# Kernel tuning notes

Measured on AMD Instinct MI355X. Metric: run time of the kernel, lower is better.

Reference implementation:

```python
import jax, jax.numpy as jnp
from jax import lax
import numpy as np

N, I, O = 64, 8, 8
B = 512
S_EX, S_PHI, S_RHO = 10, 60, 60  # S_phi must equal S_rho (alpha loops feed S_rho-sized h into the GRUs)
N_ACTIONS, N_ROLES = 5, 7


def _gru(x, h, Wih, Whh, bih, bhh):
    # torch.nn.GRUCell math
    gi = x @ Wih.T + bih
    gh = h @ Whh.T + bhh
    ir, iz, inn = jnp.split(gi, 3, axis=-1)
    hr, hz, hn = jnp.split(gh, 3, axis=-1)
    r = jax.nn.sigmoid(ir + hr)
    zg = jax.nn.sigmoid(iz + hz)
    n = jnp.tanh(inn + r * hn)
    return (1.0 - zg) * n + zg * h


def setup_inputs() -> dict:
    key = jax.random.key(0)
    ks = jax.random.split(key, 24)
    f32 = jnp.float32
    z = jax.random.normal(ks[0], (B, N, S_EX), f32)
    dz = jax.random.normal(ks[1], (B, N, S_EX), f32)
    has = (jax.random.uniform(ks[2], (B, N)) < 0.9).astype(f32)
    adj = (jnp.triu(jax.random.uniform(ks[3], (N, N)), 1) > 0.7).astype(jnp.int32)

    def lin(k, o, i):
        return (jax.random.normal(k, (o, i), f32) * np.float32(1.0 / np.sqrt(i)))

    d = dict(z=z, dz=dz, has=has, adj=adj)
    d['Wih_f'] = lin(ks[4], 3 * S_PHI, S_RHO)
    d['Whh_f'] = lin(ks[5], 3 * S_PHI, S_PHI)
    d['bih_f'] = jax.random.normal(ks[6], (3 * S_PHI,), f32) * 0.02
    d['bhh_f'] = jax.random.normal(ks[7], (3 * S_PHI,), f32) * 0.02
    d['Wih_b'] = lin(ks[8], 3 * S_PHI, S_RHO)
    d['Whh_b'] = lin(ks[9], 3 * S_PHI, S_PHI)
    d['bih_b'] = jax.random.normal(ks[10], (3 * S_PHI,), f32) * 0.02
    d['bhh_b'] = jax.random.normal(ks[11], (3 * S_PHI,), f32) * 0.02
    d['Wf'] = lin(ks[12], S_RHO, S_PHI + 2 * S_EX)
    d['bf'] = jax.random.normal(ks[13], (S_RHO,), f32) * 0.02
    d['Wb'] = lin(ks[14], S_RHO, S_PHI + 2 * S_EX)
    d['bb'] = jax.random.normal(ks[15], (S_RHO,), f32) * 0.02
    d['Wa'] = lin(ks[16], N_ACTIONS, 2 * S_PHI)
    d['ba'] = jax.random.normal(ks[17], (N_ACTIONS,), f32) * 0.02
    d['Wc'] = lin(ks[18], 1, 2 * S_PHI)
    d['bc'] = jax.random.normal(ks[19], (1,), f32) * 0.02
    d['Wu'] = lin(ks[20], N_ROLES, 2 * S_RHO)
    d['bu'] = jax.random.normal(ks[21], (N_ROLES,), f32) * 0.02
    return d


def reference(z, dz, has, adj,
              Wih_f, Whh_f, bih_f, bhh_f,
              Wih_b, Whh_b, bih_b, bhh_b,
              Wf, bf, Wb, bb, Wa, ba, Wc, bc, Wu, bu):
    Bn, Nn = has.shape
    dt = z.dtype
    adjf = adj.astype(dt)

    # ---- forward sweep over nodes in ascending order ----
    def fwd_outer(rho, i):
        def inner(h, j):
            hn = _gru(rho[j], h, Wih_f, Whh_f, bih_f, bhh_f)
            blend = adjf[j, i] * has[:, j][:, None]  # edge exists AND source node present
            return h + blend * (hn - h), None
        h, _ = lax.scan(inner, jnp.zeros((Bn, S_PHI), dt), jnp.arange(Nn))
        rho_i = jnp.tanh(jnp.concatenate([h, z[:, i], dz[:, i]], 1) @ Wf.T + bf)
        return rho.at[i].set(rho_i), None

    rho_f, _ = lax.scan(fwd_outer, jnp.zeros((Nn, Bn, S_RHO), dt), jnp.arange(Nn))

    # ---- backward sweep over nodes in descending order ----
    def bwd_outer(rho, i):
        def inner(h, j):
            hn = _gru(rho[j], h, Wih_b, Whh_b, bih_b, bhh_b)
            blend = adjf[i, j] * has[:, j][:, None]  # out-edges of i, visited descending
            return h + blend * (hn - h), None
        h, _ = lax.scan(inner, jnp.zeros((Bn, S_PHI), dt), jnp.arange(Nn - 1, -1, -1))
        rho_i = jnp.concatenate([h, z[:, i], dz[:, i]], 1) @ Wb.T + bb
        return rho.at[i].set(rho_i), None

    rho_b, _ = lax.scan(bwd_outer, jnp.zeros((Nn, Bn, S_RHO), dt), jnp.arange(Nn - 1, -1, -1))

    # ---- aggregate outputs (last O nodes) and inputs (first I nodes) ----
    h = jnp.zeros((Bn, S_RHO), dt)
    for i in range(N - O, N):
        hn = _gru(rho_f[i], h, Wih_f, Whh_f, bih_f, bhh_f)
        h = h + has[:, i][:, None] * (hn - h)
    alpha_f = h
    h = jnp.zeros((Bn, S_RHO), dt)
    for i in reversed(range(I)):
        hn = _gru(rho_b[i], h, Wih_b, Whh_b, bih_b, bhh_b)
        h = h + has[:, i][:, None] * (hn - h)
    alpha_b = h

    ab = jnp.concatenate([alpha_f, alpha_b], 1)
    omega = ab @ Wa.T + ba          # [B, 5]
    value = ab @ Wc.T + bc          # [B, 1]

    feats = jnp.concatenate([rho_f, rho_b], -1)           # [N, B, 2*S_rho]
    psi = jnp.einsum('nbs,rs->brn', feats, Wu) + bu[None, :, None]  # [B, 7, N]
    m = has[:, None, :]
    psi = -60.0 * (1.0 - m) + psi * m  # interpolate(-60, psi, has)

    instr_prob = jax.nn.softmax(omega, axis=1)
    role_prob = jax.nn.softmax(psi, axis=2)
    return instr_prob, role_prob, value
```

## Files before the change

### kernel.cpp

```cpp
#include <hip/hip_runtime.h>
#include <hip/hip_bf16.h>

#define NN 64
#define BATCH 512
#define SP 60
#define SG 180
#define SEX 10
#define CATD 80
#define NA 5
#define NR 7
#define OO 8
#define II 8

typedef unsigned long long u64;
typedef unsigned short u16;
typedef unsigned int u32;
typedef unsigned char u8;

#define OFF_Z     0
#define OFF_DZ    327680
#define OFF_HAS   655360
#define OFF_WIHF  688128
#define OFF_WHHF  698928
#define OFF_BIHF  709728
#define OFF_BHHF  709908
#define OFF_WIHB  710088
#define OFF_WHHB  720888
#define OFF_BIHB  731688
#define OFF_BHHB  731868
#define OFF_WF    732048
#define OFF_BF    736848
#define OFF_WB    736908
#define OFF_BB    741708
#define OFF_WA    741768
#define OFF_BA    742368
#define OFF_WC    742373
#define OFF_BC    742493
#define OFF_WU    742494
#define OFF_BU    743334
#define CONV_TOTAL 743341
#define OFF_FLAG  743342
#define OFF_RHOF  743344
#define OFF_RHOB  (OFF_RHOF + 1966080)
#define OFF_ALF   (OFF_RHOB + 1966080)
#define OFF_ALB   (OFF_ALF + 30720)
#define OUT_TOTAL 232448

typedef _Float16 f16;
typedef _Float16 half2_t __attribute__((ext_vector_type(2)));
typedef _Float16 f16x8 __attribute__((ext_vector_type(8)));
typedef float f32x4 __attribute__((ext_vector_type(4)));

__device__ __forceinline__ float us2f(u16 v){
  return __uint_as_float(((u32)v) << 16);
}
__device__ __forceinline__ u16 f2bf(float f){
  __hip_bfloat16 h = __float2bfloat16(f);
  return *reinterpret_cast<u16*>(&h);
}
__device__ __forceinline__ float rcp_(float x){ return __builtin_amdgcn_rcpf(x); }
__device__ __forceinline__ float sigm(float x){
  return rcp_(1.f + __expf(-x));
}
__device__ __forceinline__ float tanh_(float x){
  float e = __expf(2.f*fabsf(x));
  float t = 1.f - 2.f*rcp_(e + 1.f);
  return copysignf(t, x);
}
__device__ __forceinline__ u32 pack2(float a, float b){
  half2_t h; h[0] = (f16)a; h[1] = (f16)b;
  return __builtin_bit_cast(u32, h);
}
__device__ __forceinline__ float fdot2_(u32 a, u32 b, float c){
  return __builtin_amdgcn_fdot2(__builtin_bit_cast(half2_t, a),
                                __builtin_bit_cast(half2_t, b), c, false);
}
__device__ __forceinline__ f16x8 bc16(uint4 v){ return __builtin_bit_cast(f16x8, v); }
__device__ __forceinline__ f32x4 mfma16(f16x8 a, f16x8 b, f32x4 c){
  return __builtin_amdgcn_mfma_f32_16x16x32_f16(a, b, c, 0, 0, 0);
}

__global__ __launch_bounds__(256) void conv_in(
  const void* z, const void* dz, const void* has,
  const void* WihF, const void* WhhF, const void* bihF, const void* bhhF,
  const void* WihB, const void* WhhB, const void* bihB, const void* bhhB,
  const void* Wf_, const void* bf_, const void* Wb_, const void* bb_,
  const void* Wa, const void* ba, const void* Wc, const void* bc,
  const void* Wu, const void* bu, float* ws)
{
  __shared__ int sIsBf;
  const int tid = threadIdx.x;
  if (tid < 64){
    const u32* w = (const u32*)has;
    int f = 0;
    #pragma unroll
    for (int k=0;k<4;k++) f |= (w[tid*4 + k] == 0x3F803F80u) ? 1 : 0;
    u64 m = __ballot(f != 0);
    if (tid == 0) sIsBf = (m != 0ULL) ? 1 : 0;
  }
  __syncthreads();
  const int isbf = sIsBf;
  if (blockIdx.x == 0 && tid == 0) ws[OFF_FLAG] = (float)isbf;
  int idx = blockIdx.x*256 + tid;
  if (idx >= CONV_TOTAL) return;
  const void* src; int loc;
  if      (idx < OFF_DZ  ){ src=z;    loc=idx-OFF_Z;    }
  else if (idx < OFF_HAS ){ src=dz;   loc=idx-OFF_DZ;   }
  else if (idx < OFF_WIHF){ src=has;  loc=idx-OFF_HAS;  }
  else if (idx < OFF_WHHF){ src=WihF; loc=idx-OFF_WIHF; }
  else if (idx < OFF_BIHF){ src=WhhF; loc=idx-OFF_WHHF; }
  else if (idx < OFF_BHHF){ src=bihF; loc=idx-OFF_BIHF; }
  else if (idx < OFF_WIHB){ src=bhhF; loc=idx-OFF_BHHF; }
  else if (idx < OFF_WHHB){ src=WihB; loc=idx-OFF_WIHB; }
  else if (idx < OFF_BIHB){ src=WhhB; loc=idx-OFF_WHHB; }
  else if (idx < OFF_BHHB){ src=bihB; loc=idx-OFF_BIHB; }
  else if (idx < OFF_WF  ){ src=bhhB; loc=idx-OFF_BHHB; }
  else if (idx < OFF_BF  ){ src=Wf_;  loc=idx-OFF_WF;   }
  else if (idx < OFF_WB  ){ src=bf_;  loc=idx-OFF_BF;   }
  else if (idx < OFF_BB  ){ src=Wb_;  loc=idx-OFF_WB;   }
  else if (idx < OFF_WA  ){ src=bb_;  loc=idx-OFF_BB;   }
  else if (idx < OFF_BA  ){ src=Wa;   loc=idx-OFF_WA;   }
  else if (idx < OFF_WC  ){ src=ba;   loc=idx-OFF_BA;   }
  else if (idx < OFF_BC  ){ src=Wc;   loc=idx-OFF_WC;   }
  else if (idx < OFF_WU  ){ src=bc;   loc=idx-OFF_BC;   }
  else if (idx < OFF_BU  ){ src=Wu;   loc=idx-OFF_WU;   }
  else                    { src=bu;   loc=idx-OFF_BU;   }
  float v = isbf ? us2f(((const u16*)src)[loc]) : ((const float*)src)[loc];
  ws[idx] = v;
}

__global__ __launch_bounds__(256, 2) void dir_kernel(const int* __restrict__ adj,
                                                     float* __restrict__ ws)
{
  const int tid = threadIdx.x;
  const int w   = tid >> 6;
  const int u   = tid & 63;
  const int ml  = u & 15;
  const int q   = u >> 4;
  const int bid = blockIdx.x;
  const int bwd = bid >> 8;
  const int bp  = (bid & 255) << 1;

  const float* Wih  = ws + (bwd ? OFF_WIHB : OFF_WIHF);
  const float* Whh  = ws + (bwd ? OFF_WHHB : OFF_WHHF);
  const float* bih  = ws + (bwd ? OFF_BIHB : OFF_BIHF);
  const float* bhh  = ws + (bwd ? OFF_BHHB : OFF_BHHF);
  const float* Wcat = ws + (bwd ? OFF_WB   : OFF_WF);
  const float* bcat = ws + (bwd ? OFF_BB   : OFF_BF);
  const float* zc   = ws + OFF_Z;
  const float* dzc  = ws + OFF_DZ;
  const float* hasc = ws + OFF_HAS;
  float* rho   = ws + (bwd ? OFF_RHOB : OFF_RHOF);
  float* alpha = ws + (bwd ? OFF_ALB  : OFF_ALF);

  __shared__ uint4 sH4[2][65][9];
  __shared__ uint4 sRhoPad[2][8];
  __shared__ uint4 sRhoHist[2][8][8];
  __shared__ float sZdc[2][NN][SP];
  __shared__ u32 sZp[2][NN][5];
  __shared__ u32 sDZp[2][NN][5];
  __shared__ float sHas[2][NN];
  __shared__ u64 sRowM[NN];
  __shared__ u8 sConsL[NN][64];
  __shared__ int sConsCnt[NN];

  #define ROWB(E,I) ((char*)&sH4[(E)][(I)][0])
  const u32 BIASW = 0x3C000000u;

  {
    if (tid < 64){
      u64 rowm = 0;
      for (int j=0;j<64;j++) rowm |= ((u64)(adj[tid*64+j]!=0))<<j;
      sRowM[tid] = rowm;
    }
    if (tid < 128){
      const int e = tid >> 6, n = tid & 63;
      sHas[e][n] = hasc[(bp+e)*NN + n];
    }
    for (int idx=tid; idx<2*65*9; idx+=256){
      uint4 v = {0,0,0,0};
      if ((idx % 9) == 7) v.w = BIASW;
      ((uint4*)sH4)[idx] = v;
    }
    if (tid < 16){ uint4 v={0,0,0,0}; if ((tid&7)==7) v.w = BIASW; ((uint4*)sRhoPad)[tid]=v; }
    if (tid < 128){ uint4 v={0,0,0,0}; if ((tid&7)==7) v.w = BIASW; ((uint4*)sRhoHist)[tid]=v; }
    for (int idx=tid; idx<2*NN*5; idx+=256){
      int e = idx/(NN*5), rem = idx%(NN*5), n2=rem/5, p2=rem%5;
      sZp [e][n2][p2] = pack2(zc [(size_t)(bp+e)*NN*SEX + n2*SEX + 2*p2],
                              zc [(size_t)(bp+e)*NN*SEX + n2*SEX + 2*p2+1]);
      sDZp[e][n2][p2] = pack2(dzc[(size_t)(bp+e)*NN*SEX + n2*SEX + 2*p2],
                              dzc[(size_t)(bp+e)*NN*SEX + n2*SEX + 2*p2+1]);
    }
  }
  __syncthreads();
  if (tid < 64){
    u64 cm = 0;
    if (bwd) for (int i2=0;i2<64;i2++) cm |= ((sRowM[i2]>>tid)&1ULL)<<i2;
    u64 m = bwd ? cm : sRowM[tid];
    int c = 0;
    while (m){ int i2 = (int)__builtin_ctzll(m); m &= m-1; sConsL[tid][c++] = (u8)i2; }
    sConsCnt[tid] = c;
  }
  {
    const int uu = tid & 63;
    const int tw = tid >> 6;
    if (uu < SP){
      u32 wz[10];
      #pragma unroll
      for (int p=0;p<10;p++)
        wz[p] = pack2(Wcat[uu*CATD + 60 + 2*p], Wcat[uu*CATD + 60 + 2*p + 1]);
      const float bb0 = bcat[uu];
      for (int et=tw; et<2*NN; et+=4){
        const int e = et >> 6, t2 = et & 63;
        float c = bb0;
        #pragma unroll
        for (int p=0;p<5;p++){
          c = fdot2_(wz[p],   sZp [e][t2][p], c);
          c = fdot2_(wz[5+p], sDZp[e][t2][p], c);
        }
        sZdc[e][t2][uu] = c;
      }
    }
  }

  f16x8 Ar[4], Az[4], Anh[2], Ani[2], Ac[2];
  {
    const int R = 16*w + ml;
    const bool rok = (R < SP);
    #pragma unroll
    for (int kt=0; kt<4; kt++){
      f16x8 vr, vz;
      #pragma unroll
      for (int j=0;j<8;j++){
        const int K = 32*kt + 8*q + j;
        float wr=0.f, wz2=0.f;
        if (rok){
          if (K < SP){ wr = Whh[R*SP+K]; wz2 = Whh[(60+R)*SP+K]; }
          else if (K >= 64 && K < 64+SP){ wr = Wih[R*SP+(K-64)]; wz2 = Wih[(60+R)*SP+(K-64)]; }
          else if (K == 127){ wr = bhh[R]+bih[R]; wz2 = bhh[60+R]+bih[60+R]; }
        }
        vr[j]=(f16)wr; vz[j]=(f16)wz2;
      }
      Ar[kt]=vr; Az[kt]=vz;
    }
    #pragma unroll
    for (int kt=0; kt<2; kt++){
      f16x8 vn, vi, vc;
      #pragma unroll
      for (int j=0;j<8;j++){
        const int K = 32*kt + 8*q + j;
        float wn=0.f, wi=0.f, wcv=0.f;
        if (rok){
          if (K < SP){ wn = Whh[(120+R)*SP+K]; wi = Wih[(120+R)*SP+K]; wcv = Wcat[R*CATD+K]; }
          else if (K == 63){ wn = bhh[120+R]; wi = bih[120+R]; }
        }
        vn[j]=(f16)wn; vi[j]=(f16)wi; vc[j]=(f16)wcv;
      }
      Anh[kt]=vn; Ani[kt]=vi; Ac[kt]=vc;
    }
  }
  __syncthreads();

  auto gates = [&](f32x4 Dr, f32x4 Dz, f32x4 Dn, f32x4 Gn,
                   char* rowb, bool wr, float bl){
    char* rp = rowb + 32*w + 8*q;
    uint2 h2 = *(uint2*)rp;
    half2_t ha = __builtin_bit_cast(half2_t, h2.x);
    half2_t hb = __builtin_bit_cast(half2_t, h2.y);
    float hold[4] = { (float)ha[0], (float)ha[1], (float)hb[0], (float)hb[1] };
    float hw[4];
    #pragma unroll
    for (int reg=0;reg<4;reg++){
      float r_ = sigm(Dr[reg]);
      float zg = sigm(Dz[reg]);
      float nv = tanh_(Gn[reg] + r_*Dn[reg]);
      float hn_ = (1.f - zg)*nv + zg*hold[reg];
      hw[reg] = (bl != 0.f) ? hn_ : hold[reg];
    }
    if (wr && !(w==3 && q==3)){
      uint2 o; o.x = pack2(hw[0],hw[1]); o.y = pack2(hw[2],hw[3]);
      *(uint2*)rp = o;
    }
  };

  auto fullpass = [&](f16x8 Bh0, f16x8 Bh1, f16x8 Br0, f16x8 Br1,
                      f32x4 Gn, char* rowb, bool wr, float bl){
    f32x4 Dr={0,0,0,0}, Dz={0,0,0,0}, Dn={0,0,0,0};
    Dr = mfma16(Ar[0], Bh0, Dr); Dr = mfma16(Ar[1], Bh1, Dr);
    Dr = mfma16(Ar[2], Br0, Dr); Dr = mfma16(Ar[3], Br1, Dr);
    Dz = mfma16(Az[0], Bh0, Dz); Dz = mfma16(Az[1], Bh1, Dz);
    Dz = mfma16(Az[2], Br0, Dz); Dz = mfma16(Az[3], Br1, Dz);
    Dn = mfma16(Anh[0], Bh0, Dn); Dn = mfma16(Anh[1], Bh1, Dn);
    gates(Dr, Dz, Dn, Gn, rowb, wr, bl);
  };

  int t = bwd ? 63 : 0;
  const int dt = bwd ? -1 : 1;
  for (int s=0; s<64; s++, t+=dt){
    const int cnt = sConsCnt[t];
    const float bl0 = sHas[0][t];
    const float bl1 = sHas[1][t];
    const bool act   = (cnt > 0) && (bl0 != 0.f || bl1 != 0.f);
    const bool fastp = act && (cnt <= 8);
    const bool slowp = act && (cnt > 8);
    const bool g1    = act && (cnt > 16);

    int ci0 = 64, ci1 = 64, cim = 64;
    const int eh = ml >> 3;
    f16x8 Bm0={}, Bm1={};
    f16x8 Bh0e0={}, Bh1e0={}, Bh0e1={}, Bh1e1={};
    f16x8 Ch0e0={}, Ch1e0={}, Ch0e1={}, Ch1e1={};
    if (fastp){
      const int sl = ml & 7;
      cim = (sl < cnt) ? (int)sConsL[t][sl] : 64;
      Bm0 = bc16(sH4[eh][cim][q]);
      Bm1 = bc16(sH4[eh][cim][4+q]);
    } else if (slowp){
      ci0 = (ml < cnt) ? (int)sConsL[t][ml] : 64;
      Bh0e0 = bc16(sH4[0][ci0][q]); Bh1e0 = bc16(sH4[0][ci0][4+q]);
      Bh0e1 = bc16(sH4[1][ci0][q]); Bh1e1 = bc16(sH4[1][ci0][4+q]);
      if (g1){
        ci1 = (16 + ml < cnt) ? (int)sConsL[t][16 + ml] : 64;
        Ch0e0 = bc16(sH4[0][ci1][q]); Ch1e0 = bc16(sH4[0][ci1][4+q]);
        Ch0e1 = bc16(sH4[1][ci1][q]); Ch1e1 = bc16(sH4[1][ci1][4+q]);
      }
    }

    {
      const int em = (ml >> 2) & 1;
      const f16x8 Hm0 = bc16(sH4[em][t][q]);
      const f16x8 Hm1 = bc16(sH4[em][t][4+q]);
      f32x4 Rv = {0,0,0,0};
      Rv = mfma16(Ac[0], Hm0, Rv);
      Rv = mfma16(Ac[1], Hm1, Rv);
      const int row = 16*w + 4*q + (ml & 3);
      if (ml < 8 && row < SP){
        const int m3 = ml & 3;
        float vv = Rv[0];
        vv = (m3==1) ? Rv[1] : vv;
        vv = (m3==2) ? Rv[2] : vv;
        vv = (m3==3) ? Rv[3] : vv;
        vv += sZdc[em][t][row];
        if (!bwd) vv = tanh_(vv);
        *(f16*)((char*)&sRhoPad[em][0] + 2*row) = (f16)vv;
        const int slot = bwd ? t : (t - (NN-OO));
        if (slot >= 0 && slot < 8)
          *(f16*)((char*)&sRhoHist[em][slot][0] + 2*row) = (f16)vv;
        rho[((size_t)t*BATCH + bp + em)*SP + row] = vv;
      }
    }
    __syncthreads();

    if (fastp){
      const f16x8 Brm0 = bc16(sRhoPad[eh][q]);
      const f16x8 Brm1 = bc16(sRhoPad[eh][4+q]);
      f32x4 Gn={0,0,0,0};
      Gn = mfma16(Ani[0], Brm0, Gn); Gn = mfma16(Ani[1], Brm1, Gn);
      f32x4 Dr={0,0,0,0}, Dz={0,0,0,0}, Dn={0,0,0,0};
      Dr = mfma16(Ar[2], Brm0, Dr); Dr = mfma16(Ar[3], Brm1, Dr);
      Dr = mfma16(Ar[0], Bm0,  Dr); Dr = mfma16(Ar[1], Bm1,  Dr);
      Dz = mfma16(Az[2], Brm0, Dz); Dz = mfma16(Az[3], Brm1, Dz);
      Dz = mfma16(Az[0], Bm0,  Dz); Dz = mfma16(Az[1], Bm1,  Dz);
      Dn = mfma16(Anh[0], Bm0, Dn); Dn = mfma16(Anh[1], Bm1, Dn);
      gates(Dr, Dz, Dn, Gn, ROWB(eh, cim), (ml & 7) < cnt, eh ? bl1 : bl0);
    } else if (slowp){
      const f16x8 Br0e0 = bc16(sRhoPad[0][q]);
      const f16x8 Br1e0 = bc16(sRhoPad[0][4+q]);
      const f16x8 Br0e1 = bc16(sRhoPad[1][q]);
      const f16x8 Br1e1 = bc16(sRhoPad[1][4+q]);
      f32x4 Gn0={0,0,0,0}, Gn1={0,0,0,0};
      Gn0 = mfma16(Ani[0], Br0e0, Gn0);  Gn1 = mfma16(Ani[0], Br0e1, Gn1);
      Gn0 = mfma16(Ani[1], Br1e0, Gn0);  Gn1 = mfma16(Ani[1], Br1e1, Gn1);
      f32x4 Pr0={0,0,0,0}, Pr1={0,0,0,0};
      Pr0 = mfma16(Ar[2], Br0e0, Pr0);   Pr1 = mfma16(Ar[2], Br0e1, Pr1);
      Pr0 = mfma16(Ar[3], Br1e0, Pr0);   Pr1 = mfma16(Ar[3], Br1e1, Pr1);
      f32x4 Pz0={0,0,0,0}, Pz1={0,0,0,0};
      Pz0 = mfma16(Az[2], Br0e0, Pz0);   Pz1 = mfma16(Az[2], Br0e1, Pz1);
      Pz0 = mfma16(Az[3], Br1e0, Pz0);   Pz1 = mfma16(Az[3], Br1e1, Pz1);

      {
        f32x4 Dr0=Pr0, Dz0=Pz0, Dn0={0,0,0,0};
        f32x4 Dr1=Pr1, Dz1=Pz1, Dn1={0,0,0,0};
        Dr0 = mfma16(Ar[0], Bh0e0, Dr0);  Dr1 = mfma16(Ar[0], Bh0e1, Dr1);
        Dr0 = mfma16(Ar[1], Bh1e0, Dr0);  Dr1 = mfma16(Ar[1], Bh1e1, Dr1);
        Dz0 = mfma16(Az[0], Bh0e0, Dz0);  Dz1 = mfma16(Az[0], Bh0e1, Dz1);
        Dz0 = mfma16(Az[1], Bh1e0, Dz0);  Dz1 = mfma16(Az[1], Bh1e1, Dz1);
        Dn0 = mfma16(Anh[0], Bh0e0, Dn0); Dn1 = mfma16(Anh[0], Bh0e1, Dn1);
        Dn0 = mfma16(Anh[1], Bh1e0, Dn0); Dn1 = mfma16(Anh[1], Bh1e1, Dn1);
        gates(Dr0, Dz0, Dn0, Gn0, ROWB(0,ci0), ml < cnt, bl0);
        gates(Dr1, Dz1, Dn1, Gn1, ROWB(1,ci0), ml < cnt, bl1);
      }
      if (g1){
        f32x4 Dr0=Pr0, Dz0=Pz0, Dn0={0,0,0,0};
        f32x4 Dr1=Pr1, Dz1=Pz1, Dn1={0,0,0,0};
        Dr0 = mfma16(Ar[0], Ch0e0, Dr0);  Dr1 = mfma16(Ar[0], Ch0e1, Dr1);
        Dr0 = mfma16(Ar[1], Ch1e0, Dr0);  Dr1 = mfma16(Ar[1], Ch1e1, Dr1);
        Dz0 = mfma16(Az[0], Ch0e0, Dz0);  Dz1 = mfma16(Az[0], Ch0e1, Dz1);
        Dz0 = mfma16(Az[1], Ch1e0, Dz0);  Dz1 = mfma16(Az[1], Ch1e1, Dz1);
        Dn0 = mfma16(Anh[0], Ch0e0, Dn0); Dn1 = mfma16(Anh[0], Ch0e1, Dn1);
        Dn0 = mfma16(Anh[1], Ch1e0, Dn0); Dn1 = mfma16(Anh[1], Ch1e1, Dn1);
        gates(Dr0, Dz0, Dn0, Gn0, ROWB(0,ci1), 16 + ml < cnt, bl0);
        gates(Dr1, Dz1, Dn1, Gn1, ROWB(1,ci1), 16 + ml < cnt, bl1);
      }
      for (int p=2; 16*p < cnt; p++){
        const int idxp = 16*p + ml;
        const int ci = (idxp < cnt) ? (int)sConsL[t][idxp] : 64;
        fullpass(bc16(sH4[0][ci][q]), bc16(sH4[0][ci][4+q]),
                 Br0e0, Br1e0, Gn0, ROWB(0,ci), idxp < cnt, bl0);
        fullpass(bc16(sH4[1][ci][q]), bc16(sH4[1][ci][4+q]),
                 Br0e1, Br1e1, Gn1, ROWB(1,ci), idxp < cnt, bl1);
      }
    }
    __syncthreads();
  }

  for (int s2=0; s2<8; s2++){
    const int i = bwd ? (7 - s2) : (NN - OO + s2);
    const int slot = bwd ? i : (i - (NN-OO));
    const f16x8 Th00 = bc16(sH4[0][64][q]);
    const f16x8 Th01 = bc16(sH4[0][64][4+q]);
    const f16x8 Th10 = bc16(sH4[1][64][q]);
    const f16x8 Th11 = bc16(sH4[1][64][4+q]);
    const f16x8 Tr00 = bc16(sRhoHist[0][slot][q]);
    const f16x8 Tr01 = bc16(sRhoHist[0][slot][4+q]);
    const f16x8 Tr10 = bc16(sRhoHist[1][slot][q]);
    const f16x8 Tr11 = bc16(sRhoHist[1][slot][4+q]);
    f32x4 Gt0={0,0,0,0}, Gt1={0,0,0,0};
    Gt0 = mfma16(Ani[0], Tr00, Gt0);  Gt1 = mfma16(Ani[0], Tr10, Gt1);
    Gt0 = mfma16(Ani[1], Tr01, Gt0);  Gt1 = mfma16(Ani[1], Tr11, Gt1);
    __syncthreads();
    fullpass(Th00, Th01, Tr00, Tr01, Gt0, ROWB(0,64), ml==0, sHas[0][i]);
    fullpass(Th10, Th11, Tr10, Tr11, Gt1, ROWB(1,64), ml==0, sHas[1][i]);
    __syncthreads();
  }
  if (tid < SP){
    alpha[(size_t)(bp  )*SP + tid] = (float)*(const f16*)(ROWB(0,64) + 2*tid);
    alpha[(size_t)(bp+1)*SP + tid] = (float)*(const f16*)(ROWB(1,64) + 2*tid);
  }
  #undef ROWB
}

__global__ __launch_bounds__(256, 1) void head_kernel(float* __restrict__ ws,
                                                      void* __restrict__ outp)
{
  const int b = blockIdx.x;
  const int tid = threadIdx.x;
  const int isbf = (ws[OFF_FLAG] != 0.f);
  const float* hasc   = ws + OFF_HAS;
  const float* WaC    = ws + OFF_WA;
  const float* baC    = ws + OFF_BA;
  const float* WcC    = ws + OFF_WC;
  const float* bcC    = ws + OFF_BC;
  const float* WuC    = ws + OFF_WU;
  const float* buC    = ws + OFF_BU;
  const float* rhoF   = ws + OFF_RHOF;
  const float* rhoB   = ws + OFF_RHOB;
  const float* alphaF = ws + OFF_ALF;
  const float* alphaB = ws + OFF_ALB;

  __shared__ float sF[NN][122];
  __shared__ float sAB[120];
  __shared__ float sWu[NR*120];
  __shared__ float sHasR[NN];
  __shared__ float sPsi[NR][NN];
  __shared__ float sOm[NA];

  auto wout = [&](int idx, float v){
    if (isbf) ((u16*)outp)[idx] = f2bf(v);
    else      ((float*)outp)[idx] = v;
  };

  for (int idx=tid; idx<NN*SP; idx+=256){
    int n = idx/SP, s = idx%SP;
    sF[n][s]    = rhoF[((size_t)n*BATCH + b)*SP + s];
    sF[n][60+s] = rhoB[((size_t)n*BATCH + b)*SP + s];
  }
  for (int idx=tid; idx<120; idx+=256)
    sAB[idx] = (idx<60) ? alphaF[(size_t)b*SP + idx] : alphaB[(size_t)b*SP + idx-60];
  for (int idx=tid; idx<NR*120; idx+=256) sWu[idx] = WuC[idx];
  for (int idx=tid; idx<NN; idx+=256) sHasR[idx] = hasc[b*NN + idx];
  __syncthreads();

  for (int idx=tid; idx<NR*NN; idx+=256){
    int r = idx/NN, n = idx%NN;
    const float2* fn = (const float2*)&sF[n][0];
    const float2* wr = (const float2*)&sWu[r*120];
    float acc = buC[r];
    #pragma unroll 6
    for (int s2=0;s2<60;s2++){
      float2 a = fn[s2], c = wr[s2];
      acc += a.x*c.x;
      acc += a.y*c.y;
    }
    sPsi[r][n] = (sHasR[n] != 0.f) ? acc : -60.f;
  }
  if (tid >= 64 && tid < 64+NA){
    int a = tid - 64;
    float acc = baC[a];
    for (int s=0;s<120;s++) acc += sAB[s]*WaC[a*120+s];
    sOm[a] = acc;
  }
  if (tid == 70){
    float acc = bcC[0];
    for (int s=0;s<120;s++) acc += sAB[s]*WcC[s];
    wout(2560 + BATCH*NR*NN + b, acc);
  }
  __syncthreads();

  if (tid < NR*32){
    const int r = tid >> 5, l = tid & 31;
    float v0 = sPsi[r][l], v1 = sPsi[r][l+32];
    float m = fmaxf(v0, v1);
    #pragma unroll
    for (int o=16;o>0;o>>=1) m = fmaxf(m, __shfl_xor(m, o, 64));
    float e0 = __expf(v0 - m), e1 = __expf(v1 - m);
    float ssum = e0 + e1;
    #pragma unroll
    for (int o=16;o>0;o>>=1) ssum += __shfl_xor(ssum, o, 64);
    float rinv = 1.f/ssum;
    wout(2560 + (size_t)b*NR*NN + r*NN + l,    e0*rinv);
    wout(2560 + (size_t)b*NR*NN + r*NN + l+32, e1*rinv);
  }
  if (tid == 224){
    float m = -1e30f;
    for (int a=0;a<NA;a++) m = fmaxf(m, sOm[a]);
    float e[NA]; float ssum = 0.f;
    for (int a=0;a<NA;a++){ e[a] = __expf(sOm[a]-m); ssum += e[a]; }
    for (int a=0;a<NA;a++) wout(b*NA + a, e[a]/ssum);
  }
}

extern "C" void kernel_launch(void* const* d_in, const int* in_sizes, int n_in,
                              void* d_out, int out_size, void* d_ws, size_t ws_size,
                              hipStream_t stream)
{
  const int* adj = (const int*)d_in[3];
  float* ws = (float*)d_ws;

  conv_in<<<(CONV_TOTAL+255)/256, 256, 0, stream>>>(
      d_in[0], d_in[1], d_in[2],
      d_in[4], d_in[5], d_in[6], d_in[7],
      d_in[8], d_in[9], d_in[10], d_in[11],
      d_in[12], d_in[13], d_in[14], d_in[15],
      d_in[16], d_in[17], d_in[18], d_in[19],
      d_in[20], d_in[21], ws);

  dir_kernel<<<512, 256, 0, stream>>>(adj, ws);

  head_kernel<<<512, 256, 0, stream>>>(ws, d_out);
}
```

Baseline: 246.8 us.

## Drop conversion kernel, add single-active-batch path, halve alpha GRU MFMAs

Removes the separate conv_in launch: each kernel now detects the bf16/fp32 input type itself and reads the raw inputs with an on-the-fly conversion. In the recurrent node loop, a new path handles the case where only one of the two batch elements in a block has the node present, issuing roughly half the MFMAs of the dual path. The alpha aggregation loop packs both batch elements into one MFMA pass by splitting lanes instead of running two passes. The trade-off is redundant type detection in every block and more branch divergence and register pressure in dir_kernel.

```diff
diff --git a/kernel.cpp b/kernel.cpp
--- a/kernel.cpp
+++ b/kernel.cpp
@@ -17,34 +17,10 @@
 typedef unsigned int u32;
 typedef unsigned char u8;
 
-#define OFF_Z     0
-#define OFF_DZ    327680
-#define OFF_HAS   655360
-#define OFF_WIHF  688128
-#define OFF_WHHF  698928
-#define OFF_BIHF  709728
-#define OFF_BHHF  709908
-#define OFF_WIHB  710088
-#define OFF_WHHB  720888
-#define OFF_BIHB  731688
-#define OFF_BHHB  731868
-#define OFF_WF    732048
-#define OFF_BF    736848
-#define OFF_WB    736908
-#define OFF_BB    741708
-#define OFF_WA    741768
-#define OFF_BA    742368
-#define OFF_WC    742373
-#define OFF_BC    742493
-#define OFF_WU    742494
-#define OFF_BU    743334
-#define CONV_TOTAL 743341
-#define OFF_FLAG  743342
 #define OFF_RHOF  743344
 #define OFF_RHOB  (OFF_RHOF + 1966080)
 #define OFF_ALF   (OFF_RHOB + 1966080)
 #define OFF_ALB   (OFF_ALF + 30720)
-#define OUT_TOTAL 232448
 
 typedef _Float16 f16;
 typedef _Float16 half2_t __attribute__((ext_vector_type(2)));
@@ -79,58 +55,17 @@
 __device__ __forceinline__ f32x4 mfma16(f16x8 a, f16x8 b, f32x4 c){
   return __builtin_amdgcn_mfma_f32_16x16x32_f16(a, b, c, 0, 0, 0);
 }
-
-__global__ __launch_bounds__(256) void conv_in(
-  const void* z, const void* dz, const void* has,
-  const void* WihF, const void* WhhF, const void* bihF, const void* bhhF,
-  const void* WihB, const void* WhhB, const void* bihB, const void* bhhB,
+__device__ __forceinline__ float ldw(const void* p, size_t i, int isbf){
+  return isbf ? us2f(((const u16*)p)[i]) : ((const float*)p)[i];
+}
+
+__global__ __launch_bounds__(256, 2) void dir_kernel(
+  const int* __restrict__ adj, const void* zp_, const void* dzp_,
+  const void* hasp_,
+  const void* WihF_, const void* WhhF_, const void* bihF_, const void* bhhF_,
+  const void* WihB_, const void* WhhB_, const void* bihB_, const void* bhhB_,
   const void* Wf_, const void* bf_, const void* Wb_, const void* bb_,
-  const void* Wa, const void* ba, const void* Wc, const void* bc,
-  const void* Wu, const void* bu, float* ws)
-{
-  __shared__ int sIsBf;
-  const int tid = threadIdx.x;
-  if (tid < 64){
-    const u32* w = (const u32*)has;
-    int f = 0;
-    #pragma unroll
-    for (int k=0;k<4;k++) f |= (w[tid*4 + k] == 0x3F803F80u) ? 1 : 0;
-    u64 m = __ballot(f != 0);
-    if (tid == 0) sIsBf = (m != 0ULL) ? 1 : 0;
-  }
-  __syncthreads();
-  const int isbf = sIsBf;
-  if (blockIdx.x == 0 && tid == 0) ws[OFF_FLAG] = (float)isbf;
-  int idx = blockIdx.x*256 + tid;
-  if (idx >= CONV_TOTAL) return;
-  const void* src; int loc;
-  if      (idx < OFF_DZ  ){ src=z;    loc=idx-OFF_Z;    }
-  else if (idx < OFF_HAS ){ src=dz;   loc=idx-OFF_DZ;   }
-  else if (idx < OFF_WIHF){ src=has;  loc=idx-OFF_HAS;  }
-  else if (idx < OFF_WHHF){ src=WihF; loc=idx-OFF_WIHF; }
-  else if (idx < OFF_BIHF){ src=WhhF; loc=idx-OFF_WHHF; }
-  else if (idx < OFF_BHHF){ src=bihF; loc=idx-OFF_BIHF; }
-  else if (idx < OFF_WIHB){ src=bhhF; loc=idx-OFF_BHHF; }
-  else if (idx < OFF_WHHB){ src=WihB; loc=idx-OFF_WIHB; }
-  else if (idx < OFF_BIHB){ src=WhhB; loc=idx-OFF_WHHB; }
-  else if (idx < OFF_BHHB){ src=bihB; loc=idx-OFF_BIHB; }
-  else if (idx < OFF_WF  ){ src=bhhB; loc=idx-OFF_BHHB; }
-  else if (idx < OFF_BF  ){ src=Wf_;  loc=idx-OFF_WF;   }
-  else if (idx < OFF_WB  ){ src=bf_;  loc=idx-OFF_BF;   }
-  else if (idx < OFF_BB  ){ src=Wb_;  loc=idx-OFF_WB;   }
-  else if (idx < OFF_WA  ){ src=bb_;  loc=idx-OFF_BB;   }
-  else if (idx < OFF_BA  ){ src=Wa;   loc=idx-OFF_WA;   }
-  else if (idx < OFF_WC  ){ src=ba;   loc=idx-OFF_BA;   }
-  else if (idx < OFF_BC  ){ src=Wc;   loc=idx-OFF_WC;   }
-  else if (idx < OFF_WU  ){ src=bc;   loc=idx-OFF_BC;   }
-  else if (idx < OFF_BU  ){ src=Wu;   loc=idx-OFF_WU;   }
-  else                    { src=bu;   loc=idx-OFF_BU;   }
-  float v = isbf ? us2f(((const u16*)src)[loc]) : ((const float*)src)[loc];
-  ws[idx] = v;
-}
-
-__global__ __launch_bounds__(256, 2) void dir_kernel(const int* __restrict__ adj,
-                                                     float* __restrict__ ws)
+  float* __restrict__ ws)
 {
   const int tid = threadIdx.x;
   const int w   = tid >> 6;
@@ -141,15 +76,24 @@
   const int bwd = bid >> 8;
   const int bp  = (bid & 255) << 1;
 
-  const float* Wih  = ws + (bwd ? OFF_WIHB : OFF_WIHF);
-  const float* Whh  = ws + (bwd ? OFF_WHHB : OFF_WHHF);
-  const float* bih  = ws + (bwd ? OFF_BIHB : OFF_BIHF);
-  const float* bhh  = ws + (bwd ? OFF_BHHB : OFF_BHHF);
-  const float* Wcat = ws + (bwd ? OFF_WB   : OFF_WF);
-  const float* bcat = ws + (bwd ? OFF_BB   : OFF_BF);
-  const float* zc   = ws + OFF_Z;
-  const float* dzc  = ws + OFF_DZ;
-  const float* hasc = ws + OFF_HAS;
+  __shared__ int sIsBf;
+  if (tid < 64){
+    const u32* hw_ = (const u32*)hasp_;
+    int f = 0;
+    #pragma unroll
+    for (int k=0;k<4;k++) f |= (hw_[tid*4 + k] == 0x3F803F80u) ? 1 : 0;
+    u64 m = __ballot(f != 0);
+    if (tid == 0) sIsBf = (m != 0ULL) ? 1 : 0;
+  }
+  __syncthreads();
+  const int isbf = sIsBf;
+
+  const void* Wihp  = bwd ? WihB_ : WihF_;
+  const void* Whhp  = bwd ? WhhB_ : WhhF_;
+  const void* bihp  = bwd ? bihB_ : bihF_;
+  const void* bhhp  = bwd ? bhhB_ : bhhF_;
+  const void* Wcatp = bwd ? Wb_   : Wf_;
+  const void* bcatp = bwd ? bb_   : bf_;
   float* rho   = ws + (bwd ? OFF_RHOB : OFF_RHOF);
   float* alpha = ws + (bwd ? OFF_ALB  : OFF_ALF);
 
@@ -175,7 +119,7 @@
     }
     if (tid < 128){
       const int e = tid >> 6, n = tid & 63;
-      sHas[e][n] = hasc[(bp+e)*NN + n];
+      sHas[e][n] = ldw(hasp_, (size_t)(bp+e)*NN + n, isbf);
     }
     for (int idx=tid; idx<2*65*9; idx+=256){
       uint4 v = {0,0,0,0};
@@ -186,10 +130,9 @@
     if (tid < 128){ uint4 v={0,0,0,0}; if ((tid&7)==7) v.w = BIASW; ((uint4*)sRhoHist)[tid]=v; }
     for (int idx=tid; idx<2*NN*5; idx+=256){
       int e = idx/(NN*5), rem = idx%(NN*5), n2=rem/5, p2=rem%5;
-      sZp [e][n2][p2] = pack2(zc [(size_t)(bp+e)*NN*SEX + n2*SEX + 2*p2],
-                              zc [(size_t)(bp+e)*NN*SEX + n2*SEX + 2*p2+1]);
-      sDZp[e][n2][p2] = pack2(dzc[(size_t)(bp+e)*NN*SEX + n2*SEX + 2*p2],
-                              dzc[(size_t)(bp+e)*NN*SEX + n2*SEX + 2*p2+1]);
+      const size_t base = (size_t)(bp+e)*NN*SEX + n2*SEX + 2*p2;
+      sZp [e][n2][p2] = pack2(ldw(zp_,  base, isbf), ldw(zp_,  base+1, isbf));
+      sDZp[e][n2][p2] = pack2(ldw(dzp_, base, isbf), ldw(dzp_, base+1, isbf));
     }
   }
   __syncthreads();
@@ -208,8 +151,9 @@
       u32 wz[10];
       #pragma unroll
       for (int p=0;p<10;p++)
-        wz[p] = pack2(Wcat[uu*CATD + 60 + 2*p], Wcat[uu*CATD + 60 + 2*p + 1]);
-      const float bb0 = bcat[uu];
+        wz[p] = pack2(ldw(Wcatp, uu*CATD + 60 + 2*p,     isbf),
+                      ldw(Wcatp, uu*CATD + 60 + 2*p + 1, isbf));
+      const float bb0 = ldw(bcatp, uu, isbf);
       for (int et=tw; et<2*NN; et+=4){
         const int e = et >> 6, t2 = et & 63;
         float c = bb0;
@@ -235,9 +179,9 @@
         const int K = 32*kt + 8*q + j;
         float wr=0.f, wz2=0.f;
         if (rok){
-          if (K < SP){ wr = Whh[R*SP+K]; wz2 = Whh[(60+R)*SP+K]; }
-          else if (K >= 64 && K < 64+SP){ wr = Wih[R*SP+(K-64)]; wz2 = Wih[(60+R)*SP+(K-64)]; }
-          else if (K == 127){ wr = bhh[R]+bih[R]; wz2 = bhh[60+R]+bih[60+R]; }
+          if (K < SP){ wr = ldw(Whhp, R*SP+K, isbf); wz2 = ldw(Whhp, (60+R)*SP+K, isbf); }
+          else if (K >= 64 && K < 64+SP){ wr = ldw(Wihp, R*SP+(K-64), isbf); wz2 = ldw(Wihp, (60+R)*SP+(K-64), isbf); }
+          else if (K == 127){ wr = ldw(bhhp,R,isbf)+ldw(bihp,R,isbf); wz2 = ldw(bhhp,60+R,isbf)+ldw(bihp,60+R,isbf); }
         }
         vr[j]=(f16)wr; vz[j]=(f16)wz2;
       }
@@ -251,8 +195,8 @@
         const int K = 32*kt + 8*q + j;
         float wn=0.f, wi=0.f, wcv=0.f;
         if (rok){
-          if (K < SP){ wn = Whh[(120+R)*SP+K]; wi = Wih[(120+R)*SP+K]; wcv = Wcat[R*CATD+K]; }
-          else if (K == 63){ wn = bhh[120+R]; wi = bih[120+R]; }
+          if (K < SP){ wn = ldw(Whhp,(120+R)*SP+K,isbf); wi = ldw(Wihp,(120+R)*SP+K,isbf); wcv = ldw(Wcatp,R*CATD+K,isbf); }
+          else if (K == 63){ wn = ldw(bhhp,120+R,isbf); wi = ldw(bihp,120+R,isbf); }
         }
         vn[j]=(f16)wn; vi[j]=(f16)wi; vc[j]=(f16)wcv;
       }
@@ -300,14 +244,21 @@
     const int cnt = sConsCnt[t];
     const float bl0 = sHas[0][t];
     const float bl1 = sHas[1][t];
-    const bool act   = (cnt > 0) && (bl0 != 0.f || bl1 != 0.f);
-    const bool fastp = act && (cnt <= 8);
-    const bool slowp = act && (cnt > 8);
-    const bool g1    = act && (cnt > 16);
+    const bool a0 = (bl0 != 0.f), a1 = (bl1 != 0.f);
+    const int nact = (int)a0 + (int)a1;
+    const bool act   = (cnt > 0) && (nact > 0);
+    const bool fastp = act && (nact == 2) && (cnt <= 8);
+    const bool snglp = act && (nact == 1);
+    const bool dualp = act && (nact == 2) && (cnt > 8);
+    const bool g1d   = dualp && (cnt > 16);
+    const bool g1s   = snglp && (cnt > 16);
+    const int  ea    = a0 ? 0 : 1;
+    const float bla  = a0 ? bl0 : bl1;
 
     int ci0 = 64, ci1 = 64, cim = 64;
     const int eh = ml >> 3;
     f16x8 Bm0={}, Bm1={};
+    f16x8 B0a={}, B1a={}, C0a={}, C1a={};
     f16x8 Bh0e0={}, Bh1e0={}, Bh0e1={}, Bh1e1={};
     f16x8 Ch0e0={}, Ch1e0={}, Ch0e1={}, Ch1e1={};
     if (fastp){
@@ -315,11 +266,18 @@
       cim = (sl < cnt) ? (int)sConsL[t][sl] : 64;
       Bm0 = bc16(sH4[eh][cim][q]);
       Bm1 = bc16(sH4[eh][cim][4+q]);
-    } else if (slowp){
+    } else if (snglp){
+      ci0 = (ml < cnt) ? (int)sConsL[t][ml] : 64;
+      B0a = bc16(sH4[ea][ci0][q]); B1a = bc16(sH4[ea][ci0][4+q]);
+      if (g1s){
+        ci1 = (16 + ml < cnt) ? (int)sConsL[t][16 + ml] : 64;
+        C0a = bc16(sH4[ea][ci1][q]); C1a = bc16(sH4[ea][ci1][4+q]);
+      }
+    } else if (dualp){
       ci0 = (ml < cnt) ? (int)sConsL[t][ml] : 64;
       Bh0e0 = bc16(sH4[0][ci0][q]); Bh1e0 = bc16(sH4[0][ci0][4+q]);
       Bh0e1 = bc16(sH4[1][ci0][q]); Bh1e1 = bc16(sH4[1][ci0][4+q]);
-      if (g1){
+      if (g1d){
         ci1 = (16 + ml < cnt) ? (int)sConsL[t][16 + ml] : 64;
         Ch0e0 = bc16(sH4[0][ci1][q]); Ch1e0 = bc16(sH4[0][ci1][4+q]);
         Ch0e1 = bc16(sH4[1][ci1][q]); Ch1e1 = bc16(sH4[1][ci1][4+q]);
@@ -363,7 +321,36 @@
       Dz = mfma16(Az[0], Bm0,  Dz); Dz = mfma16(Az[1], Bm1,  Dz);
       Dn = mfma16(Anh[0], Bm0, Dn); Dn = mfma16(Anh[1], Bm1, Dn);
       gates(Dr, Dz, Dn, Gn, ROWB(eh, cim), (ml & 7) < cnt, eh ? bl1 : bl0);
-    } else if (slowp){
+    } else if (snglp){
+      const f16x8 Br0 = bc16(sRhoPad[ea][q]);
+      const f16x8 Br1 = bc16(sRhoPad[ea][4+q]);
+      f32x4 Gn={0,0,0,0};
+      Gn = mfma16(Ani[0], Br0, Gn); Gn = mfma16(Ani[1], Br1, Gn);
+      f32x4 Pr={0,0,0,0};
+      Pr = mfma16(Ar[2], Br0, Pr); Pr = mfma16(Ar[3], Br1, Pr);
+      f32x4 Pz={0,0,0,0};
+      Pz = mfma16(Az[2], Br0, Pz); Pz = mfma16(Az[3], Br1, Pz);
+      {
+        f32x4 Dr=Pr, Dz=Pz, Dn={0,0,0,0};
+        Dr = mfma16(Ar[0], B0a, Dr);  Dr = mfma16(Ar[1], B1a, Dr);
+        Dz = mfma16(Az[0], B0a, Dz);  Dz = mfma16(Az[1], B1a, Dz);
+        Dn = mfma16(Anh[0], B0a, Dn); Dn = mfma16(Anh[1], B1a, Dn);
+        gates(Dr, Dz, Dn, Gn, ROWB(ea,ci0), ml < cnt, bla);
+      }
+      if (g1s){
+        f32x4 Dr=Pr, Dz=Pz, Dn={0,0,0,0};
+        Dr = mfma16(Ar[0], C0a, Dr);  Dr = mfma16(Ar[1], C1a, Dr);
+        Dz = mfma16(Az[0], C0a, Dz);  Dz = mfma16(Az[1], C1a, Dz);
+        Dn = mfma16(Anh[0], C0a, Dn); Dn = mfma16(Anh[1], C1a, Dn);
+        gates(Dr, Dz, Dn, Gn, ROWB(ea,ci1), 16 + ml < cnt, bla);
+      }
+      for (int p=2; 16*p < cnt; p++){
+        const int idxp = 16*p + ml;
+        const int ci = (idxp < cnt) ? (int)sConsL[t][idxp] : 64;
+        fullpass(bc16(sH4[ea][ci][q]), bc16(sH4[ea][ci][4+q]),
+                 Br0, Br1, Gn, ROWB(ea,ci), idxp < cnt, bla);
+      }
+    } else if (dualp){
       const f16x8 Br0e0 = bc16(sRhoPad[0][q]);
       const f16x8 Br1e0 = bc16(sRhoPad[0][4+q]);
       const f16x8 Br0e1 = bc16(sRhoPad[1][q]);
@@ -390,7 +377,7 @@
         gates(Dr0, Dz0, Dn0, Gn0, ROWB(0,ci0), ml < cnt, bl0);
         gates(Dr1, Dz1, Dn1, Gn1, ROWB(1,ci0), ml < cnt, bl1);
       }
-      if (g1){
+      if (g1d){
         f32x4 Dr0=Pr0, Dz0=Pz0, Dn0={0,0,0,0};
         f32x4 Dr1=Pr1, Dz1=Pz1, Dn1={0,0,0,0};
         Dr0 = mfma16(Ar[0], Ch0e0, Dr0);  Dr1 = mfma16(Ar[0], Ch0e1, Dr1);
@@ -417,20 +404,17 @@
   for (int s2=0; s2<8; s2++){
     const int i = bwd ? (7 - s2) : (NN - OO + s2);
     const int slot = bwd ? i : (i - (NN-OO));
-    const f16x8 Th00 = bc16(sH4[0][64][q]);
-    const f16x8 Th01 = bc16(sH4[0][64][4+q]);
-    const f16x8 Th10 = bc16(sH4[1][64][q]);
-    const f16x8 Th11 = bc16(sH4[1][64][4+q]);
-    const f16x8 Tr00 = bc16(sRhoHist[0][slot][q]);
-    const f16x8 Tr01 = bc16(sRhoHist[0][slot][4+q]);
-    const f16x8 Tr10 = bc16(sRhoHist[1][slot][q]);
-    const f16x8 Tr11 = bc16(sRhoHist[1][slot][4+q]);
-    f32x4 Gt0={0,0,0,0}, Gt1={0,0,0,0};
-    Gt0 = mfma16(Ani[0], Tr00, Gt0);  Gt1 = mfma16(Ani[0], Tr10, Gt1);
-    Gt0 = mfma16(Ani[1], Tr01, Gt0);  Gt1 = mfma16(Ani[1], Tr11, Gt1);
+    const int et = ml >> 3;
+    const f16x8 Th0 = bc16(sH4[et][64][q]);
+    const f16x8 Th1 = bc16(sH4[et][64][4+q]);
+    const f16x8 Tr0 = bc16(sRhoHist[et][slot][q]);
+    const f16x8 Tr1 = bc16(sRhoHist[et][slot][4+q]);
+    f32x4 Gt={0,0,0,0};
+    Gt = mfma16(Ani[0], Tr0, Gt);
+    Gt = mfma16(Ani[1], Tr1, Gt);
     __syncthreads();
-    fullpass(Th00, Th01, Tr00, Tr01, Gt0, ROWB(0,64), ml==0, sHas[0][i]);
-    fullpass(Th10, Th11, Tr10, Tr11, Gt1, ROWB(1,64), ml==0, sHas[1][i]);
+    fullpass(Th0, Th1, Tr0, Tr1, Gt, ROWB(et,64), (ml&7)==0,
+             et ? sHas[1][i] : sHas[0][i]);
     __syncthreads();
   }
   if (tid < SP){
@@ -440,19 +424,26 @@
   #undef ROWB
 }
 
-__global__ __launch_bounds__(256, 1) void head_kernel(float* __restrict__ ws,
-                                                      void* __restrict__ outp)
+__global__ __launch_bounds__(256, 1) void head_kernel(
+  const void* hasp_, const void* Wa_, const void* ba_, const void* Wc_,
+  const void* bc_, const void* Wu_, const void* bu_,
+  float* __restrict__ ws, void* __restrict__ outp)
 {
   const int b = blockIdx.x;
   const int tid = threadIdx.x;
-  const int isbf = (ws[OFF_FLAG] != 0.f);
-  const float* hasc   = ws + OFF_HAS;
-  const float* WaC    = ws + OFF_WA;
-  const float* baC    = ws + OFF_BA;
-  const float* WcC    = ws + OFF_WC;
-  const float* bcC    = ws + OFF_BC;
-  const float* WuC    = ws + OFF_WU;
-  const float* buC    = ws + OFF_BU;
+
+  __shared__ int sIsBf;
+  if (tid < 64){
+    const u32* hw_ = (const u32*)hasp_;
+    int f = 0;
+    #pragma unroll
+    for (int k=0;k<4;k++) f |= (hw_[tid*4 + k] == 0x3F803F80u) ? 1 : 0;
+    u64 m = __ballot(f != 0);
+    if (tid == 0) sIsBf = (m != 0ULL) ? 1 : 0;
+  }
+  __syncthreads();
+  const int isbf = sIsBf;
+
   const float* rhoF   = ws + OFF_RHOF;
   const float* rhoB   = ws + OFF_RHOB;
   const float* alphaF = ws + OFF_ALF;
@@ -477,15 +468,15 @@
   }
   for (int idx=tid; idx<120; idx+=256)
     sAB[idx] = (idx<60) ? alphaF[(size_t)b*SP + idx] : alphaB[(size_t)b*SP + idx-60];
-  for (int idx=tid; idx<NR*120; idx+=256) sWu[idx] = WuC[idx];
-  for (int idx=tid; idx<NN; idx+=256) sHasR[idx] = hasc[b*NN + idx];
+  for (int idx=tid; idx<NR*120; idx+=256) sWu[idx] = ldw(Wu_, idx, isbf);
+  for (int idx=tid; idx<NN; idx+=256) sHasR[idx] = ldw(hasp_, (size_t)b*NN + idx, isbf);
   __syncthreads();
 
   for (int idx=tid; idx<NR*NN; idx+=256){
     int r = idx/NN, n = idx%NN;
     const float2* fn = (const float2*)&sF[n][0];
     const float2* wr = (const float2*)&sWu[r*120];
-    float acc = buC[r];
+    float acc = ldw(bu_, r, isbf);
     #pragma unroll 6
     for (int s2=0;s2<60;s2++){
       float2 a = fn[s2], c = wr[s2];
@@ -496,13 +487,13 @@
   }
   if (tid >= 64 && tid < 64+NA){
     int a = tid - 64;
-    float acc = baC[a];
-    for (int s=0;s<120;s++) acc += sAB[s]*WaC[a*120+s];
+    float acc = ldw(ba_, a, isbf);
+    for (int s=0;s<120;s++) acc += sAB[s]*ldw(Wa_, a*120+s, isbf);
     sOm[a] = acc;
   }
   if (tid == 70){
-    float acc = bcC[0];
-    for (int s=0;s<120;s++) acc += sAB[s]*WcC[s];
+    float acc = ldw(bc_, 0, isbf);
+    for (int s=0;s<120;s++) acc += sAB[s]*ldw(Wc_, s, isbf);
     wout(2560 + BATCH*NR*NN + b, acc);
   }
   __syncthreads();
@@ -537,15 +528,13 @@
   const int* adj = (const int*)d_in[3];
   float* ws = (float*)d_ws;
 
-  conv_in<<<(CONV_TOTAL+255)/256, 256, 0, stream>>>(
-      d_in[0], d_in[1], d_in[2],
+  dir_kernel<<<512, 256, 0, stream>>>(
+      adj, d_in[0], d_in[1], d_in[2],
       d_in[4], d_in[5], d_in[6], d_in[7],
       d_in[8], d_in[9], d_in[10], d_in[11],
-      d_in[12], d_in[13], d_in[14], d_in[15],
-      d_in[16], d_in[17], d_in[18], d_in[19],
-      d_in[20], d_in[21], ws);
-
-  dir_kernel<<<512, 256, 0, stream>>>(adj, ws);
-
-  head_kernel<<<512, 256, 0, stream>>>(ws, d_out);
-}
+      d_in[12], d_in[13], d_in[14], d_in[15], ws);
+
+  head_kernel<<<512, 256, 0, stream>>>(
+      d_in[2], d_in[16], d_in[17], d_in[18], d_in[19],
+      d_in[20], d_in[21], ws, d_out);
+}
```

Result: no change. 250.4 us, median of 2 (+1.5%).
